# Performance work log

Hardware: AMD Instinct MI355X
Metric: run time of the kernel (lower is better)

The kernel has to match this reference:

```python
import jax, jax.numpy as jnp
import numpy as np

T, H, I, E, K = 4096, 2048, 768, 64, 8  # tokens, hidden, moe_intermediate, experts, top_k


def setup_inputs() -> dict:
    key = jax.random.key(0)
    k1, k2, k3, k4 = jax.random.split(key, 4)
    return {
        "x": jax.random.normal(k1, (T, H), jnp.float32),
        "gate_w": jax.random.normal(k2, (E, H), jnp.float32) * 0.02,          # router weight [E, H]
        "w_gate_up": jax.random.normal(k3, (E, H, 2 * I), jnp.float32) * 0.02,  # stacked gate|up [E, H, 2I]
        "w_down": jax.random.normal(k4, (E, I, H), jnp.float32) * 0.02,        # stacked down [E, I, H]
        "top_k": K,
    }


def reference(x, gate_w, w_gate_up, w_down, top_k):
    n_tok, hidden = x.shape
    n_exp = gate_w.shape[0]
    inter = w_down.shape[1]

    # Router: softmax over experts (fp32 for stability), top-k, renormalize (norm_topk_prob)
    logits = x @ gate_w.T                                   # [T, E]
    probs = jax.nn.softmax(logits.astype(jnp.float32), axis=-1)
    top_p, top_i = jax.lax.top_k(probs, top_k)              # [T, K]
    top_p = top_p / jnp.sum(top_p, axis=-1, keepdims=True)

    # Scatter top-k weights into dense combine matrix [T, E] (top_k indices are distinct)
    combine = jnp.zeros((n_tok, n_exp), jnp.float32)
    combine = combine.at[jnp.arange(n_tok)[:, None], top_i].set(top_p)
    combine = combine.astype(x.dtype)

    # Per-expert SwiGLU MLP, accumulated via scan over the (fixed) expert axis.
    def body(acc, ws):
        wgu, wd, cw = ws                                    # [H,2I], [I,H], [T]
        gu = x @ wgu                                        # [T, 2I]
        h = jax.nn.silu(gu[:, :inter]) * gu[:, inter:]      # [T, I]
        return acc + (h @ wd) * cw[:, None], None

    out, _ = jax.lax.scan(body, jnp.zeros_like(x), (w_gate_up, w_down, combine.T))
    return out
```

## Files before the change

kernel.cpp:

```cpp
#include <hip/hip_runtime.h>
#include <hip/hip_bf16.h>
#include <cstdint>
#include <cstddef>

#define T_TOK 4096
#define HID   2048
#define INTER 768
#define NEXP  64

typedef float  f32x4  __attribute__((ext_vector_type(4)));
typedef __bf16 bf16x8 __attribute__((ext_vector_type(8)));
typedef __bf16 bf16x4 __attribute__((ext_vector_type(4)));

__device__ __forceinline__ void gl16(const void* g, void* l) {
  __builtin_amdgcn_global_load_lds((const __attribute__((address_space(1))) void*)g,
                                   (__attribute__((address_space(3))) void*)l, 16, 0, 0);
}

#define BAR() do { asm volatile("" ::: "memory"); __builtin_amdgcn_s_barrier(); asm volatile("" ::: "memory"); } while (0)


__global__ void zero_meta_kernel(int* counts, int* fill) {
  int t = threadIdx.x;
  if (t < NEXP) { counts[t] = 0; fill[t] = 0; }
}

__global__ void scan_kernel(const int* __restrict__ counts, int* __restrict__ offsets,
                            int* __restrict__ tb) {
  if (threadIdx.x == 0) {
    int s = 0, ts = 0;
    for (int e = 0; e < NEXP; e++) {
      offsets[e] = s; tb[e] = ts;
      s += counts[e]; ts += (counts[e] + 255) >> 8;
    }
    offsets[NEXP] = s; tb[NEXP] = ts;
  }
}

__global__ void scatter_kernel(const int* __restrict__ topk_id, const float* __restrict__ topk_w,
                               const int* __restrict__ offsets, int* __restrict__ fill,
                               int* __restrict__ pair_tok, float* __restrict__ pair_w,
                               int* __restrict__ pair_pos) {
  int i = blockIdx.x * 256 + threadIdx.x;
  int e = topk_id[i];
  int pos = offsets[e] + atomicAdd(&fill[e], 1);
  pair_tok[pos] = i >> 3;
  pair_w[pos]  = topk_w[i];
  pair_pos[i]  = pos;
}


__device__ __forceinline__ void transpose_tile(
    const float* __restrict__ src, __bf16* __restrict__ dst,
    int Kd, int Nd, int mode, int wid, char* Sw, int lane) {
  const int g = lane >> 4, nq = lane & 15;
  const int NT = Nd >> 6, KT = Kd >> 6, NB = Nd >> 7;
  int tpe = KT * NT;
  int e = wid / tpe;
  int rem = wid - e * tpe;
  int kt = rem / NT;
  int nt = rem - kt * NT;
  const float* sp = src + ((size_t)e * Kd + (size_t)kt * 64) * Nd + nt * 64;

  float4 vv[16];
  #pragma unroll
  for (int kq = 0; kq < 16; kq++)
    vv[kq] = *(const float4*)(sp + (size_t)(kq * 4 + g) * Nd + nq * 4);

  const int n_l = nq * 4 + g;
  #pragma unroll
  for (int kq = 0; kq < 16; kq++) {
    float4 v = vv[kq];
    float t0 = __shfl_xor(v.x, 32), t1 = __shfl_xor(v.y, 32);
    float t2 = __shfl_xor(v.z, 32), t3 = __shfl_xor(v.w, 32);
    bool hi2 = (g & 2) != 0;
    float a0 = hi2 ? t2 : v.x, a1 = hi2 ? t3 : v.y;
    float a2 = hi2 ? v.z : t0, a3 = hi2 ? v.w : t1;
    float s0 = __shfl_xor(a0, 16), s1 = __shfl_xor(a1, 16);
    float s2 = __shfl_xor(a2, 16), s3 = __shfl_xor(a3, 16);
    bool odd = (g & 1) != 0;
    float u0 = odd ? s1 : a0, u1 = odd ? a1 : s0;
    float u2 = odd ? s3 : a2, u3 = odd ? a3 : s2;
    bf16x4 b; b[0] = (__bf16)u0; b[1] = (__bf16)u1; b[2] = (__bf16)u2; b[3] = (__bf16)u3;
    *(bf16x4*)(Sw + n_l * 128 + ((kq ^ (n_l & 15)) << 3)) = b;
  }
  asm volatile("s_waitcnt lgkmcnt(0)" ::: "memory");
  __builtin_amdgcn_sched_barrier(0);

  if (mode == 0) {
    uint4* gdst = (uint4*)dst + ((((size_t)e * NB + (nt >> 1)) * KT + kt) << 10) + ((nt & 1) << 6) + lane;
    #pragma unroll
    for (int q = 0; q < 8; q++) {
      int p0 = (2 * q) ^ (lane & 15), p1 = (2 * q + 1) ^ (lane & 15);
      uint2 lo = *(const uint2*)(Sw + lane * 128 + (p0 << 3));
      uint2 hi = *(const uint2*)(Sw + lane * 128 + (p1 << 3));
      gdst[q * 128] = make_uint4(lo.x, lo.y, hi.x, hi.y);
    }
  } else {
    int n = nt * 64 + lane;
    int isup = (n >= INTER) ? 1 : 0;
    int hcol = isup ? n - INTER : n;
    int nb = hcol >> 7, ho = hcol & 127;
    int rp = isup * 128 + ho;
    uint4* gdst = (uint4*)dst + ((((size_t)e * 6 + nb) * KT + kt) << 11) + rp;
    #pragma unroll
    for (int q = 0; q < 8; q++) {
      int p0 = (2 * q) ^ (lane & 15), p1 = (2 * q + 1) ^ (lane & 15);
      uint2 lo = *(const uint2*)(Sw + lane * 128 + (p0 << 3));
      uint2 hi = *(const uint2*)(Sw + lane * 128 + (p1 << 3));
      gdst[q * 256] = make_uint4(lo.x, lo.y, hi.x, hi.y);
    }
  }
}


__global__ __launch_bounds__(256) void fat1_kernel(
    const float* __restrict__ x, const float* __restrict__ gw, __bf16* __restrict__ xbf,
    int* __restrict__ topk_id, float* __restrict__ topk_w, int* __restrict__ counts,
    const float* __restrict__ wgu, __bf16* __restrict__ w2gu) {
  __shared__ __align__(16) char fsm[32768];
  const int tid = threadIdx.x, lane = tid & 63, wv = tid >> 6;

  if (blockIdx.x >= 256) {
    transpose_tile(wgu, w2gu, HID, 2 * INTER, 1,
                   ((int)blockIdx.x - 256) * 4 + wv, fsm + wv * 8192, lane);
    return;
  }

  float (*gs)[65] = (float (*)[65])fsm;
  float (*xs)[65] = (float (*)[65])(fsm + 16640);
  const int tblk = blockIdx.x * 16;

  float acc[4] = {0.f, 0.f, 0.f, 0.f};
  for (int kc = 0; kc < HID; kc += 64) {
    #pragma unroll
    for (int i = 0; i < 4; i++) {
      int r = tid >> 2;
      int c = (tid & 3) * 16 + i * 4;
      float4 v = *(const float4*)(gw + (size_t)r * HID + kc + c);
      gs[r][c + 0] = v.x; gs[r][c + 1] = v.y; gs[r][c + 2] = v.z; gs[r][c + 3] = v.w;
    }
    {
      int r = tid >> 4;
      int c = (tid & 15) * 4;
      float4 v = *(const float4*)(x + (size_t)(tblk + r) * HID + kc + c);
      xs[r][c + 0] = v.x; xs[r][c + 1] = v.y; xs[r][c + 2] = v.z; xs[r][c + 3] = v.w;
      bf16x4 b;
      b[0] = (__bf16)v.x; b[1] = (__bf16)v.y; b[2] = (__bf16)v.z; b[3] = (__bf16)v.w;
      *(bf16x4*)(xbf + (size_t)(tblk + r) * HID + kc + c) = b;
    }
    __syncthreads();
    #pragma unroll 8
    for (int k = 0; k < 64; k++) {
      float g = gs[lane][k];
      #pragma unroll
      for (int j = 0; j < 4; j++) acc[j] = fmaf(xs[wv * 4 + j][k], g, acc[j]);
    }
    __syncthreads();
  }

  for (int j = 0; j < 4; j++) {
    int t = tblk + wv * 4 + j;
    float vsel = acc[j];
    float m1 = 0.f, denom = 0.f;
    int myid = 0; float myw = 0.f;
    for (int s = 0; s < 8; s++) {
      float bv = vsel; int bi = lane;
      #pragma unroll
      for (int off = 32; off > 0; off >>= 1) {
        float ov = __shfl_xor(bv, off);
        int   oi = __shfl_xor(bi, off);
        if (ov > bv || (ov == bv && oi < bi)) { bv = ov; bi = oi; }
      }
      if (s == 0) m1 = bv;
      float ev = __expf(bv - m1);
      denom += ev;
      if (lane == s)  { myid = bi; myw = ev; }
      if (lane == bi) vsel = -3.402823466e38f;
    }
    if (lane < 8) {
      topk_id[t * 8 + lane] = myid;
      topk_w[t * 8 + lane]  = myw / denom;
      atomicAdd(&counts[myid], 1);
    }
  }
}


__global__ __launch_bounds__(512, 2) void fat2_kernel(
    const uint4* __restrict__ xbf4, const uint4* __restrict__ w2gu,
    const int* __restrict__ offsets, const int* __restrict__ tb,
    const int* __restrict__ pair_tok, const float* __restrict__ pair_w,
    uint4* __restrict__ H2,
    const float* __restrict__ wd, __bf16* __restrict__ w2d, int nwgG1) {
  __shared__ __align__(16) char smem[163840];
  const int tid = threadIdx.x, lane = tid & 63, w = tid >> 6;
  const int bid = blockIdx.x;

  if (bid >= nwgG1) {
    transpose_tile(wd, w2d, INTER, HID, 0,
                   (bid - nwgG1) * 8 + w, smem + w * 8192, lane);
    return;
  }

  const int q8 = nwgG1 >> 3, r8 = nwgG1 & 7;
  const int xcd = bid & 7, idx = bid >> 3;
  const int wg = (xcd < r8 ? xcd * (q8 + 1) : r8 * (q8 + 1) + (xcd - r8) * q8) + idx;
  const int mt0 = wg % 3, t1 = wg / 3, nb = t1 % 6, e = t1 / 6;
  const int off = offsets[e], cnt = offsets[e + 1] - off;
  const uint4* Bb = w2gu + (size_t)(e * 6 + nb) * 65536;
  const int wm = w >> 2, wn = w & 3;
  const int g = lane >> 4, nq = lane & 15;

#define STA1(s, ks) do {                                                         \
    char* d_ = smem + (s) * 32768 + (w << 12);                                   \
    gl16(a0b + (size_t)(ks) * 8, d_ + (lane << 4));                              \
    gl16(a1b + (size_t)(ks) * 8, d_ + ((128 + lane) << 4)); } while (0)
#define STA2(s, ks) do {                                                         \
    char* d_ = smem + (s) * 32768 + (w << 12);                                   \
    gl16(a2b + (size_t)(ks) * 8, d_ + ((64 + lane) << 4));                       \
    gl16(a3b + (size_t)(ks) * 8, d_ + ((192 + lane) << 4)); } while (0)
#define STBG(pb, ks) do { size_t so_ = (size_t)(ks) * 2048 + (w << 8);           \
    char* d_ = smem + 98304 + (pb) * 32768 + (w << 12);                          \
    gl16(Bb + so_ + lane,       d_ + (lane << 4));                               \
    gl16(Bb + so_ + 64 + lane,  d_ + ((64 + lane) << 4)); } while (0)
#define STBU(pb, ks) do { size_t so_ = (size_t)(ks) * 2048 + (w << 8);           \
    char* d_ = smem + 98304 + (pb) * 32768 + (w << 12);                          \
    gl16(Bb + so_ + 128 + lane, d_ + ((128 + lane) << 4));                       \
    gl16(Bb + so_ + 192 + lane, d_ + ((192 + lane) << 4)); } while (0)

  for (int mt = mt0; mt * 256 < cnt; mt += 3) {
    const int rows = min(256, cnt - mt * 256);
    const int m0 = mt * 256;
    const int rm = rows - 1;
    const uint4* a0b = xbf4 + (size_t)pair_tok[off + m0 + min(lane, rm)]       * 256 + w;
    const uint4* a1b = xbf4 + (size_t)pair_tok[off + m0 + min(128 + lane, rm)] * 256 + w;
    const uint4* a2b = xbf4 + (size_t)pair_tok[off + m0 + min(64 + lane, rm)]  * 256 + w;
    const uint4* a3b = xbf4 + (size_t)pair_tok[off + m0 + min(192 + lane, rm)] * 256 + w;

    f32x4 ag[8][2], au[8][2];
    #pragma unroll
    for (int i = 0; i < 8; i++)
      #pragma unroll
      for (int j = 0; j < 2; j++)
        #pragma unroll
        for (int q = 0; q < 4; q++) { ag[i][j][q] = 0.f; au[i][j][q] = 0.f; }

    STA1(0, 0); STA2(0, 0); STBG(0, 0); STBU(0, 0); STA1(1, 1); STA2(1, 1);
    for (int ks = 0; ks < 32; ks++) {
      char* bA = smem + (ks % 3) * 32768;
      const int pb = ks & 1;
      char* bB = smem + 98304 + pb * 32768;
      bf16x8 af[4][2], bg[2][2], bu[2][2];
      if (ks < 31) asm volatile("s_waitcnt vmcnt(6)" ::: "memory");
      else         asm volatile("s_waitcnt vmcnt(2)" ::: "memory");
      BAR();
      if (ks + 1 < 32) STBG(pb ^ 1, ks + 1);
      #pragma unroll
      for (int kk = 0; kk < 2; kk++) {
        const int q = kk * 4 + g;
        #pragma unroll
        for (int mi = 0; mi < 4; mi++)
          af[mi][kk] = *(const bf16x8*)(bA + (q << 12) + ((wm * 128 + mi * 16 + nq) << 4));
        #pragma unroll
        for (int ni = 0; ni < 2; ni++)
          bg[ni][kk] = *(const bf16x8*)(bB + (q << 12) + ((wn * 32 + ni * 16 + nq) << 4));
      }
      __builtin_amdgcn_s_setprio(1);
      #pragma unroll
      for (int kk = 0; kk < 2; kk++)
        #pragma unroll
        for (int mi = 0; mi < 4; mi++)
          #pragma unroll
          for (int ni = 0; ni < 2; ni++)
            ag[mi][ni] = __builtin_amdgcn_mfma_f32_16x16x32_bf16(af[mi][kk], bg[ni][kk], ag[mi][ni], 0, 0, 0);
      __builtin_amdgcn_s_setprio(0);
      if (ks < 31) asm volatile("s_waitcnt vmcnt(6)" ::: "memory");
      else         asm volatile("s_waitcnt vmcnt(0)" ::: "memory");
      BAR();
      if (ks + 1 < 32) STBU(pb ^ 1, ks + 1);
      #pragma unroll
      for (int kk = 0; kk < 2; kk++) {
        const int q = kk * 4 + g;
        #pragma unroll
        for (int ni = 0; ni < 2; ni++)
          bu[ni][kk] = *(const bf16x8*)(bB + (q << 12) + ((128 + wn * 32 + ni * 16 + nq) << 4));
      }
      __builtin_amdgcn_s_setprio(1);
      #pragma unroll
      for (int kk = 0; kk < 2; kk++)
        #pragma unroll
        for (int mi = 0; mi < 4; mi++)
          #pragma unroll
          for (int ni = 0; ni < 2; ni++)
            au[mi][ni] = __builtin_amdgcn_mfma_f32_16x16x32_bf16(af[mi][kk], bu[ni][kk], au[mi][ni], 0, 0, 0);
      __builtin_amdgcn_s_setprio(0);
      BAR();
      if (ks + 2 < 32) STA1((ks + 2) % 3, ks + 2);
      #pragma unroll
      for (int kk = 0; kk < 2; kk++) {
        const int q = kk * 4 + g;
        #pragma unroll
        for (int mi = 0; mi < 4; mi++)
          af[mi][kk] = *(const bf16x8*)(bA + (q << 12) + ((wm * 128 + 64 + mi * 16 + nq) << 4));
      }
      __builtin_amdgcn_s_setprio(1);
      #pragma unroll
      for (int kk = 0; kk < 2; kk++)
        #pragma unroll
        for (int mi = 0; mi < 4; mi++)
          #pragma unroll
          for (int ni = 0; ni < 2; ni++)
            ag[4 + mi][ni] = __builtin_amdgcn_mfma_f32_16x16x32_bf16(af[mi][kk], bg[ni][kk], ag[4 + mi][ni], 0, 0, 0);
      __builtin_amdgcn_s_setprio(0);
      BAR();
      if (ks + 2 < 32) STA2((ks + 2) % 3, ks + 2);
      __builtin_amdgcn_s_setprio(1);
      #pragma unroll
      for (int kk = 0; kk < 2; kk++)
        #pragma unroll
        for (int mi = 0; mi < 4; mi++)
          #pragma unroll
          for (int ni = 0; ni < 2; ni++)
            au[4 + mi][ni] = __builtin_amdgcn_mfma_f32_16x16x32_bf16(af[mi][kk], bu[ni][kk], au[4 + mi][ni], 0, 0, 0);
      __builtin_amdgcn_s_setprio(0);
    }

    #pragma unroll
    for (int mi = 0; mi < 8; mi++) {
      const int mrow = (mi < 4) ? (wm * 128 + mi * 16) : (wm * 128 + 64 + (mi - 4) * 16);
      #pragma unroll
      for (int reg = 0; reg < 4; reg++) {
        int rrow = mrow + g * 4 + reg;
        float pw = (rrow < rows) ? pair_w[off + m0 + rrow] : 0.f;
        #pragma unroll
        for (int ni = 0; ni < 2; ni++) {
          float gv = ag[mi][ni][reg];
          float uv = au[mi][ni][reg];
          float sv = gv / (1.f + __expf(-gv));
          int col = wn * 32 + ni * 16 + nq;
          *(__bf16*)(smem + rrow * 256 + ((col * 2) ^ ((rrow & 7) << 4))) = (__bf16)(sv * uv * pw);
        }
      }
    }
    BAR();
    {
      uint4* Hb = H2 + (size_t)(tb[e] + mt) * 24576 + nb * 16 * 256;
      #pragma unroll
      for (int i = 0; i < 8; i++) {
        int idx2 = tid + i * 512;
        int gx = idx2 >> 8, row = idx2 & 255;
        uint4 v = *(const uint4*)(smem + row * 256 + ((gx * 16) ^ ((row & 7) << 4)));
        Hb[gx * 256 + row] = v;
      }
    }
    BAR();
  }
#undef STA1
#undef STA2
#undef STBG
#undef STBU
}


__global__ __launch_bounds__(512, 2) void gemm2_kernel(
    const uint4* __restrict__ H2, const uint4* __restrict__ w2d,
    const int* __restrict__ offsets, const int* __restrict__ tb,
    __bf16* __restrict__ ybuf, int e0, int nwg) {
  __shared__ __align__(16) char smem[131072];
  const int bid = blockIdx.x;
  const int q8 = nwg >> 3, r8 = nwg & 7;
  const int xcd = bid & 7, idx = bid >> 3;
  const int wg = (xcd < r8 ? xcd * (q8 + 1) : r8 * (q8 + 1) + (xcd - r8) * q8) + idx;
  const int mt0 = wg % 3, t1 = wg / 3, nb2 = t1 % 8, ez = t1 / 8;
  const int e = e0 + ez;
  const int off = offsets[e], cnt = offsets[e + 1] - off;
  const uint4* Bw = w2d;
  const int pnl0 = ez * 16 + nb2 * 2, pnl1 = pnl0 + 1;
  const int tid = threadIdx.x, lane = tid & 63, w = tid >> 6;
  const int wm = w >> 2, wn = w & 3;
  const int g = lane >> 4, nq = lane & 15;

#define S2A1(p, ks) do { size_t so_ = (size_t)(ks) * 2048 + (w << 8);            \
    char* d_ = smem + (p) * 65536 + (w << 12);                                   \
    gl16(Ab + so_ + lane,       d_ + (lane << 4));                               \
    gl16(Ab + so_ + 128 + lane, d_ + ((128 + lane) << 4)); } while (0)
#define S2A2(p, ks) do { size_t so_ = (size_t)(ks) * 2048 + (w << 8);            \
    char* d_ = smem + (p) * 65536 + (w << 12);                                   \
    gl16(Ab + so_ + 64 + lane,  d_ + ((64 + lane) << 4));                        \
    gl16(Ab + so_ + 192 + lane, d_ + ((192 + lane) << 4)); } while (0)
#define S2BG(p, ks) do { size_t so_ = ((size_t)pnl0 * 12 + (ks)) * 1024 + (w << 7); \
    char* d_ = smem + (p) * 65536 + 32768 + (w << 12);                           \
    gl16(Bw + so_ + lane,      d_ + (lane << 4));                                \
    gl16(Bw + so_ + 64 + lane, d_ + ((64 + lane) << 4)); } while (0)
#define S2BH(p, ks) do { size_t so_ = ((size_t)pnl1 * 12 + (ks)) * 1024 + (w << 7); \
    char* d_ = smem + (p) * 65536 + 32768 + (w << 12);                           \
    gl16(Bw + so_ + lane,      d_ + ((128 + lane) << 4));                        \
    gl16(Bw + so_ + 64 + lane, d_ + ((192 + lane) << 4)); } while (0)

  for (int mt = mt0; mt * 256 < cnt; mt += 3) {
    const int rows = min(256, cnt - mt * 256);
    const uint4* Ab = H2 + (size_t)(tb[e] + mt) * 24576;

    f32x4 a0[8][2], a1[8][2];
    #pragma unroll
    for (int i = 0; i < 8; i++)
      #pragma unroll
      for (int j = 0; j < 2; j++)
        #pragma unroll
        for (int q = 0; q < 4; q++) { a0[i][j][q] = 0.f; a1[i][j][q] = 0.f; }

    S2A1(0, 0); S2BG(0, 0); S2BH(0, 0); S2A2(0, 0);
    for (int ks = 0; ks < 12; ks++) {
      const int p = ks & 1;
      char* bA = smem + p * 65536;
      char* bB = bA + 32768;
      const bool pre = (ks + 1 < 12);
      bf16x8 af[4][2], bl[2][2], bh[2][2];
      asm volatile("s_waitcnt vmcnt(4)" ::: "memory");
      BAR();
      if (pre) S2A1(p ^ 1, ks + 1);
      #pragma unroll
      for (int kk = 0; kk < 2; kk++) {
        const int q = kk * 4 + g;
        #pragma unroll
        for (int mi = 0; mi < 4; mi++)
          af[mi][kk] = *(const bf16x8*)(bA + (q << 12) + ((wm * 128 + mi * 16 + nq) << 4));
        #pragma unroll
        for (int ni = 0; ni < 2; ni++)
          bl[ni][kk] = *(const bf16x8*)(bB + (q << 12) + ((wn * 32 + ni * 16 + nq) << 4));
      }
      __builtin_amdgcn_s_setprio(1);
      #pragma unroll
      for (int kk = 0; kk < 2; kk++)
        #pragma unroll
        for (int mi = 0; mi < 4; mi++)
          #pragma unroll
          for (int ni = 0; ni < 2; ni++)
            a0[mi][ni] = __builtin_amdgcn_mfma_f32_16x16x32_bf16(af[mi][kk], bl[ni][kk], a0[mi][ni], 0, 0, 0);
      __builtin_amdgcn_s_setprio(0);
      if (pre) asm volatile("s_waitcnt vmcnt(4)" ::: "memory");
      else     asm volatile("s_waitcnt vmcnt(2)" ::: "memory");
      BAR();
      if (pre) S2BG(p ^ 1, ks + 1);
      #pragma unroll
      for (int kk = 0; kk < 2; kk++) {
        const int q = kk * 4 + g;
        #pragma unroll
        for (int ni = 0; ni < 2; ni++)
          bh[ni][kk] = *(const bf16x8*)(bB + (q << 12) + ((128 + wn * 32 + ni * 16 + nq) << 4));
      }
      __builtin_amdgcn_s_setprio(1);
      #pragma unroll
      for (int kk = 0; kk < 2; kk++)
        #pragma unroll
        for (int mi = 0; mi < 4; mi++)
          #pragma unroll
          for (int ni = 0; ni < 2; ni++)
            a1[mi][ni] = __builtin_amdgcn_mfma_f32_16x16x32_bf16(af[mi][kk], bh[ni][kk], a1[mi][ni], 0, 0, 0);
      __builtin_amdgcn_s_setprio(0);
      if (pre) asm volatile("s_waitcnt vmcnt(4)" ::: "memory");
      else     asm volatile("s_waitcnt vmcnt(0)" ::: "memory");
      BAR();
      if (pre) S2BH(p ^ 1, ks + 1);
      #pragma unroll
      for (int kk = 0; kk < 2; kk++) {
        const int q = kk * 4 + g;
        #pragma unroll
        for (int mi = 0; mi < 4; mi++)
          af[mi][kk] = *(const bf16x8*)(bA + (q << 12) + ((wm * 128 + 64 + mi * 16 + nq) << 4));
      }
      __builtin_amdgcn_s_setprio(1);
      #pragma unroll
      for (int kk = 0; kk < 2; kk++)
        #pragma unroll
        for (int mi = 0; mi < 4; mi++)
          #pragma unroll
          for (int ni = 0; ni < 2; ni++)
            a0[4 + mi][ni] = __builtin_amdgcn_mfma_f32_16x16x32_bf16(af[mi][kk], bl[ni][kk], a0[4 + mi][ni], 0, 0, 0);
      __builtin_amdgcn_s_setprio(0);
      BAR();
      if (pre) S2A2(p ^ 1, ks + 1);
      __builtin_amdgcn_s_setprio(1);
      #pragma unroll
      for (int kk = 0; kk < 2; kk++)
        #pragma unroll
        for (int mi = 0; mi < 4; mi++)
          #pragma unroll
          for (int ni = 0; ni < 2; ni++)
            a1[4 + mi][ni] = __builtin_amdgcn_mfma_f32_16x16x32_bf16(af[mi][kk], bh[ni][kk], a1[4 + mi][ni], 0, 0, 0);
      __builtin_amdgcn_s_setprio(0);
    }

    const int m0 = mt * 256;
    #pragma unroll
    for (int mi = 0; mi < 8; mi++) {
      const int mrow = (mi < 4) ? (wm * 128 + mi * 16) : (wm * 128 + 64 + (mi - 4) * 16);
      #pragma unroll
      for (int reg = 0; reg < 4; reg++) {
        int rrow = mrow + g * 4 + reg;
        if (rrow < rows) {
          __bf16* yrow = ybuf + (size_t)(off + m0 + rrow) * HID + nb2 * 256 + wn * 32;
          #pragma unroll
          for (int ni = 0; ni < 2; ni++) {
            yrow[ni * 16 + nq]       = (__bf16)a0[mi][ni][reg];
            yrow[128 + ni * 16 + nq] = (__bf16)a1[mi][ni][reg];
          }
        }
      }
    }
  }
#undef S2A1
#undef S2A2
#undef S2BG
#undef S2BH
}


__global__ __launch_bounds__(256) void reduce_kernel(
    const __bf16* __restrict__ ybuf, const int* __restrict__ pair_pos,
    float* __restrict__ out) {
  const int t = blockIdx.x, j = threadIdx.x;
  const int* pp = pair_pos + t * 8;
  float s[8] = {0.f, 0.f, 0.f, 0.f, 0.f, 0.f, 0.f, 0.f};
  #pragma unroll
  for (int k = 0; k < 8; k++) {
    bf16x8 v = *(const bf16x8*)(ybuf + (size_t)pp[k] * HID + j * 8);
    #pragma unroll
    for (int c = 0; c < 8; c++) s[c] += (float)v[c];
  }
  float4 o0 = make_float4(s[0], s[1], s[2], s[3]);
  float4 o1 = make_float4(s[4], s[5], s[6], s[7]);
  *(float4*)(out + (size_t)t * HID + j * 8) = o0;
  *(float4*)(out + (size_t)t * HID + j * 8 + 4) = o1;
}


extern "C" void kernel_launch(void* const* d_in, const int* in_sizes, int n_in,
                              void* d_out, int out_size, void* d_ws, size_t ws_size,
                              hipStream_t stream) {
  const float* x   = (const float*)d_in[0];
  const float* gw  = (const float*)d_in[1];
  const float* wgu = (const float*)d_in[2];
  const float* wd  = (const float*)d_in[3];
  float* out = (float*)d_out;

  char* ws = (char*)d_ws;
  int*   counts   = (int*)(ws + 0);
  int*   fill     = (int*)(ws + 256);
  int*   offsets  = (int*)(ws + 512);
  int*   tb       = (int*)(ws + 1024);
  int*   topk_id  = (int*)(ws + 4096);
  float* topk_w   = (float*)(ws + 135168);
  int*   pair_tok = (int*)(ws + 266240);
  float* pair_w   = (float*)(ws + 397312);
  int*   pair_pos = (int*)(ws + 528384);
  __bf16* xbf  = (__bf16*)(ws + 1048576);
  __bf16* ybuf = (__bf16*)(ws + 68157440);
  uint4*  H2   = (uint4*)(ws + 537919488);
  const size_t w2_base = 613416960ull;
  __bf16* w2gu = (__bf16*)(ws + w2_base);
  __bf16* w2d  = (__bf16*)(ws + w2_base + 64ull * 6291456ull);

  zero_meta_kernel<<<1, 128, 0, stream>>>(counts, fill);
  fat1_kernel<<<256 + 12288, 256, 0, stream>>>(x, gw, xbf, topk_id, topk_w, counts, wgu, w2gu);
  scan_kernel<<<1, 64, 0, stream>>>(counts, offsets, tb);
  scatter_kernel<<<128, 256, 0, stream>>>(topk_id, topk_w, offsets, fill, pair_tok, pair_w, pair_pos);

  fat2_kernel<<<1152 + 3072, 512, 0, stream>>>((const uint4*)xbf, (const uint4*)w2gu,
                                               offsets, tb, pair_tok, pair_w, H2,
                                               wd, w2d, 1152);
  gemm2_kernel<<<1536, 512, 0, stream>>>(H2, (const uint4*)w2d, offsets, tb, ybuf, 0, 1536);
  reduce_kernel<<<T_TOK, 256, 0, stream>>>(ybuf, pair_pos, out);
}
```

Measured before the change: 949.2 us.

## Halve gate-up GEMM K-step and LDS footprint to fit more workgroups per CU

The fused gate/up grouped GEMM now stages 32-wide K slices instead of 64-wide, which halves the shared-memory buffers to 80 KB and doubles the K-loop trip count to 64. The per-wave load mapping is reworked so each wave issues one 16-byte global-to-LDS load per stage. The launch bound is raised to four blocks per CU, aiming at higher occupancy and better latency hiding. The cost is twice as many barriers and waitcnt points per tile. The tighter launch bound also caps VGPRs while 128 fp32 accumulators stay live per thread, which risks register spills.

After: 3.353 ms. 3.53x slower.

```diff
diff --git a/kernel.cpp b/kernel.cpp
--- a/kernel.cpp
+++ b/kernel.cpp
@@ -187,13 +187,13 @@
 }
 
 
-__global__ __launch_bounds__(512, 2) void fat2_kernel(
+__global__ __launch_bounds__(512, 4) void fat2_kernel(
     const uint4* __restrict__ xbf4, const uint4* __restrict__ w2gu,
     const int* __restrict__ offsets, const int* __restrict__ tb,
     const int* __restrict__ pair_tok, const float* __restrict__ pair_w,
     uint4* __restrict__ H2,
     const float* __restrict__ wd, __bf16* __restrict__ w2d, int nwgG1) {
-  __shared__ __align__(16) char smem[163840];
+  __shared__ __align__(16) char smem[81920];
   const int tid = threadIdx.x, lane = tid & 63, w = tid >> 6;
   const int bid = blockIdx.x;
 
@@ -211,32 +211,25 @@
   const uint4* Bb = w2gu + (size_t)(e * 6 + nb) * 65536;
   const int wm = w >> 2, wn = w & 3;
   const int g = lane >> 4, nq = lane & 15;
-
-#define STA1(s, ks) do {                                                         \
-    char* d_ = smem + (s) * 32768 + (w << 12);                                   \
-    gl16(a0b + (size_t)(ks) * 8, d_ + (lane << 4));                              \
-    gl16(a1b + (size_t)(ks) * 8, d_ + ((128 + lane) << 4)); } while (0)
-#define STA2(s, ks) do {                                                         \
-    char* d_ = smem + (s) * 32768 + (w << 12);                                   \
-    gl16(a2b + (size_t)(ks) * 8, d_ + ((64 + lane) << 4));                       \
-    gl16(a3b + (size_t)(ks) * 8, d_ + ((192 + lane) << 4)); } while (0)
-#define STBG(pb, ks) do { size_t so_ = (size_t)(ks) * 2048 + (w << 8);           \
-    char* d_ = smem + 98304 + (pb) * 32768 + (w << 12);                          \
-    gl16(Bb + so_ + lane,       d_ + (lane << 4));                               \
-    gl16(Bb + so_ + 64 + lane,  d_ + ((64 + lane) << 4)); } while (0)
-#define STBU(pb, ks) do { size_t so_ = (size_t)(ks) * 2048 + (w << 8);           \
-    char* d_ = smem + 98304 + (pb) * 32768 + (w << 12);                          \
-    gl16(Bb + so_ + 128 + lane, d_ + ((128 + lane) << 4));                       \
-    gl16(Bb + so_ + 192 + lane, d_ + ((192 + lane) << 4)); } while (0)
+  const int sq = w >> 1, sr = w & 1;
+  const int aoff  = (sq << 12) + (sr << 11);
+  const int boffg = (sq << 8) + (sr << 6);
+
+#define STA1(s, ks) gl16(rA1 + (size_t)(ks) * 4, smem + (s) * 16384 + aoff + (lane << 4))
+#define STA2(s, ks) gl16(rA2 + (size_t)(ks) * 4, smem + (s) * 16384 + aoff + 1024 + (lane << 4))
+#define STBG(pb, ks) gl16(Bb + (size_t)(ks) * 1024 + boffg + lane, \
+                          smem + 49152 + (pb) * 16384 + (boffg << 4) + (lane << 4))
+#define STBU(pb, ks) gl16(Bb + (size_t)(ks) * 1024 + boffg + 128 + lane, \
+                          smem + 49152 + (pb) * 16384 + ((boffg + 128) << 4) + (lane << 4))
 
   for (int mt = mt0; mt * 256 < cnt; mt += 3) {
     const int rows = min(256, cnt - mt * 256);
     const int m0 = mt * 256;
     const int rm = rows - 1;
-    const uint4* a0b = xbf4 + (size_t)pair_tok[off + m0 + min(lane, rm)]       * 256 + w;
-    const uint4* a1b = xbf4 + (size_t)pair_tok[off + m0 + min(128 + lane, rm)] * 256 + w;
-    const uint4* a2b = xbf4 + (size_t)pair_tok[off + m0 + min(64 + lane, rm)]  * 256 + w;
-    const uint4* a3b = xbf4 + (size_t)pair_tok[off + m0 + min(192 + lane, rm)] * 256 + w;
+    const int tok1 = pair_tok[off + m0 + min(sr * 128 + lane, rm)];
+    const int tok2 = pair_tok[off + m0 + min(sr * 128 + 64 + lane, rm)];
+    const uint4* rA1 = xbf4 + (size_t)tok1 * 256 + sq;
+    const uint4* rA2 = xbf4 + (size_t)tok2 * 256 + sq;
 
     f32x4 ag[8][2], au[8][2];
     #pragma unroll
@@ -247,82 +240,61 @@
         for (int q = 0; q < 4; q++) { ag[i][j][q] = 0.f; au[i][j][q] = 0.f; }
 
     STA1(0, 0); STA2(0, 0); STBG(0, 0); STBU(0, 0); STA1(1, 1); STA2(1, 1);
-    for (int ks = 0; ks < 32; ks++) {
-      char* bA = smem + (ks % 3) * 32768;
-      const int pb = ks & 1;
-      char* bB = smem + 98304 + pb * 32768;
-      bf16x8 af[4][2], bg[2][2], bu[2][2];
-      if (ks < 31) asm volatile("s_waitcnt vmcnt(6)" ::: "memory");
-      else         asm volatile("s_waitcnt vmcnt(2)" ::: "memory");
-      BAR();
-      if (ks + 1 < 32) STBG(pb ^ 1, ks + 1);
-      #pragma unroll
-      for (int kk = 0; kk < 2; kk++) {
-        const int q = kk * 4 + g;
-        #pragma unroll
-        for (int mi = 0; mi < 4; mi++)
-          af[mi][kk] = *(const bf16x8*)(bA + (q << 12) + ((wm * 128 + mi * 16 + nq) << 4));
+    for (int ks = 0; ks < 64; ks++) {
+      char* bA = smem + (ks % 3) * 16384;
+      char* bB = smem + 49152 + (ks & 1) * 16384;
+      bf16x8 af[4], bg[2], bu[2];
+      if (ks < 63) asm volatile("s_waitcnt vmcnt(3)" ::: "memory");
+      else         asm volatile("s_waitcnt vmcnt(1)" ::: "memory");
+      BAR();
+      if (ks + 1 < 64) STBG((ks + 1) & 1, ks + 1);
+      #pragma unroll
+      for (int mi = 0; mi < 4; mi++)
+        af[mi] = *(const bf16x8*)(bA + (g << 12) + ((wm * 128 + mi * 16 + nq) << 4));
+      #pragma unroll
+      for (int ni = 0; ni < 2; ni++)
+        bg[ni] = *(const bf16x8*)(bB + (g << 12) + ((wn * 32 + ni * 16 + nq) << 4));
+      __builtin_amdgcn_s_setprio(1);
+      #pragma unroll
+      for (int mi = 0; mi < 4; mi++)
         #pragma unroll
         for (int ni = 0; ni < 2; ni++)
-          bg[ni][kk] = *(const bf16x8*)(bB + (q << 12) + ((wn * 32 + ni * 16 + nq) << 4));
-      }
-      __builtin_amdgcn_s_setprio(1);
-      #pragma unroll
-      for (int kk = 0; kk < 2; kk++)
-        #pragma unroll
-        for (int mi = 0; mi < 4; mi++)
-          #pragma unroll
-          for (int ni = 0; ni < 2; ni++)
-            ag[mi][ni] = __builtin_amdgcn_mfma_f32_16x16x32_bf16(af[mi][kk], bg[ni][kk], ag[mi][ni], 0, 0, 0);
-      __builtin_amdgcn_s_setprio(0);
-      if (ks < 31) asm volatile("s_waitcnt vmcnt(6)" ::: "memory");
+          ag[mi][ni] = __builtin_amdgcn_mfma_f32_16x16x32_bf16(af[mi], bg[ni], ag[mi][ni], 0, 0, 0);
+      __builtin_amdgcn_s_setprio(0);
+      if (ks < 63) asm volatile("s_waitcnt vmcnt(3)" ::: "memory");
       else         asm volatile("s_waitcnt vmcnt(0)" ::: "memory");
       BAR();
-      if (ks + 1 < 32) STBU(pb ^ 1, ks + 1);
-      #pragma unroll
-      for (int kk = 0; kk < 2; kk++) {
-        const int q = kk * 4 + g;
+      if (ks + 1 < 64) STBU((ks + 1) & 1, ks + 1);
+      #pragma unroll
+      for (int ni = 0; ni < 2; ni++)
+        bu[ni] = *(const bf16x8*)(bB + (g << 12) + ((128 + wn * 32 + ni * 16 + nq) << 4));
+      __builtin_amdgcn_s_setprio(1);
+      #pragma unroll
+      for (int mi = 0; mi < 4; mi++)
         #pragma unroll
         for (int ni = 0; ni < 2; ni++)
-          bu[ni][kk] = *(const bf16x8*)(bB + (q << 12) + ((128 + wn * 32 + ni * 16 + nq) << 4));
-      }
-      __builtin_amdgcn_s_setprio(1);
-      #pragma unroll
-      for (int kk = 0; kk < 2; kk++)
-        #pragma unroll
-        for (int mi = 0; mi < 4; mi++)
-          #pragma unroll
-          for (int ni = 0; ni < 2; ni++)
-            au[mi][ni] = __builtin_amdgcn_mfma_f32_16x16x32_bf16(af[mi][kk], bu[ni][kk], au[mi][ni], 0, 0, 0);
-      __builtin_amdgcn_s_setprio(0);
-      BAR();
-      if (ks + 2 < 32) STA1((ks + 2) % 3, ks + 2);
-      #pragma unroll
-      for (int kk = 0; kk < 2; kk++) {
-        const int q = kk * 4 + g;
-        #pragma unroll
-        for (int mi = 0; mi < 4; mi++)
-          af[mi][kk] = *(const bf16x8*)(bA + (q << 12) + ((wm * 128 + 64 + mi * 16 + nq) << 4));
-      }
-      __builtin_amdgcn_s_setprio(1);
-      #pragma unroll
-      for (int kk = 0; kk < 2; kk++)
-        #pragma unroll
-        for (int mi = 0; mi < 4; mi++)
-          #pragma unroll
-          for (int ni = 0; ni < 2; ni++)
-            ag[4 + mi][ni] = __builtin_amdgcn_mfma_f32_16x16x32_bf16(af[mi][kk], bg[ni][kk], ag[4 + mi][ni], 0, 0, 0);
-      __builtin_amdgcn_s_setprio(0);
-      BAR();
-      if (ks + 2 < 32) STA2((ks + 2) % 3, ks + 2);
-      __builtin_amdgcn_s_setprio(1);
-      #pragma unroll
-      for (int kk = 0; kk < 2; kk++)
-        #pragma unroll
-        for (int mi = 0; mi < 4; mi++)
-          #pragma unroll
-          for (int ni = 0; ni < 2; ni++)
-            au[4 + mi][ni] = __builtin_amdgcn_mfma_f32_16x16x32_bf16(af[mi][kk], bu[ni][kk], au[4 + mi][ni], 0, 0, 0);
+          au[mi][ni] = __builtin_amdgcn_mfma_f32_16x16x32_bf16(af[mi], bu[ni], au[mi][ni], 0, 0, 0);
+      __builtin_amdgcn_s_setprio(0);
+      BAR();
+      if (ks + 2 < 64) STA1((ks + 2) % 3, ks + 2);
+      #pragma unroll
+      for (int mi = 0; mi < 4; mi++)
+        af[mi] = *(const bf16x8*)(bA + (g << 12) + ((wm * 128 + 64 + mi * 16 + nq) << 4));
+      __builtin_amdgcn_s_setprio(1);
+      #pragma unroll
+      for (int mi = 0; mi < 4; mi++)
+        #pragma unroll
+        for (int ni = 0; ni < 2; ni++)
+          ag[4 + mi][ni] = __builtin_amdgcn_mfma_f32_16x16x32_bf16(af[mi], bg[ni], ag[4 + mi][ni], 0, 0, 0);
+      __builtin_amdgcn_s_setprio(0);
+      BAR();
+      if (ks + 2 < 64) STA2((ks + 2) % 3, ks + 2);
+      __builtin_amdgcn_s_setprio(1);
+      #pragma unroll
+      for (int mi = 0; mi < 4; mi++)
+        #pragma unroll
+        for (int ni = 0; ni < 2; ni++)
+          au[4 + mi][ni] = __builtin_amdgcn_mfma_f32_16x16x32_bf16(af[mi], bu[ni], au[4 + mi][ni], 0, 0, 0);
       __builtin_amdgcn_s_setprio(0);
     }
 
```
